# Kernel optimization log

Hardware: AMD Instinct MI355X
Metric: run time of the kernel (lower is better)

Reference implementation:

```python
import jax, jax.numpy as jnp
import numpy as np

SIZE = 11
SIGMA = 1.5
PAD = 5

def _window2d():
    # cv2.getGaussianKernel(11, 1.5): normalized 1D Gaussian, outer product -> 2D window
    x = np.arange(SIZE) - (SIZE - 1) / 2.0
    g = np.exp(-(x * x) / (2.0 * SIGMA * SIGMA))
    g = g / g.sum()
    return jnp.asarray(np.outer(g, g), dtype=jnp.float32)

def _gconv(x, w):
    # x: [H, W]; replicate ('edge') pad by 5 then valid 11x11 correlation (matches torch
    # Conv2d with padding_mode='replicate'); output [H, W]
    xp = jnp.pad(x, PAD, mode='edge')[None, None]  # [1,1,H+10,W+10]
    y = jax.lax.conv_general_dilated(
        xp, w[None, None], window_strides=(1, 1), padding='VALID',
        dimension_numbers=('NCHW', 'OIHW', 'NCHW'))
    return y[0, 0]

def setup_inputs() -> dict:
    key = jax.random.key(0)
    k1, k2 = jax.random.split(key)
    H = W = 4096
    img1 = jax.random.uniform(k1, (H, W), dtype=jnp.float32) * 255.0
    img2 = jax.random.uniform(k2, (H, W), dtype=jnp.float32) * 255.0
    return {"img1": img1, "img2": img2}

def reference(img1, img2):
    w = _window2d()
    C1 = (0.01 * 255) ** 2
    C2 = (0.03 * 255) ** 2
    mu1 = _gconv(img1, w)
    mu2 = _gconv(img2, w)
    mu1_sq = mu1 * mu1
    mu2_sq = mu2 * mu2
    mu1_mu2 = mu1 * mu2
    sigma1_sq = _gconv(img1 * img1, w) - mu1_sq
    sigma2_sq = _gconv(img2 * img2, w) - mu2_sq
    sigma12 = _gconv(img1 * img2, w) - mu1_mu2
    ssim_map = (2 * mu1_mu2 + C1) * (2 * sigma12 + C2) / (
        (mu1_sq + mu2_sq + C1) * (sigma1_sq + sigma2_sq + C2))
    return jnp.mean(ssim_map)
```

## Files before the change

kernel.cpp:

```cpp
#include <hip/hip_runtime.h>
#include <cmath>

#define IMG_H 4096
#define IMG_W 4096
#define GX 8
#define GY 128
#define TCOLS 512
#define WCOLS 128
#define R 32
#define NITER (R + 10)
#define GOUT ((NITER + 10) / 11)
#define SWORDS_W 144
#define NF4W 36
#define NSLOTW (2*NF4W)

struct GW { float w[11]; };

__device__ __forceinline__ int clampi(int v, int lo, int hi) {
  return v < lo ? lo : (v > hi ? hi : v);
}

__global__ __launch_bounds__(256, 2) void ssim_sweep_kernel(
    const float* __restrict__ img1, const float* __restrict__ img2,
    float* __restrict__ partial, GW gw) {
  __shared__ __align__(16) float sbuf[4][2][2][SWORDS_W];

  const int tid  = threadIdx.x;
  const int wv   = tid >> 6;
  const int lane = tid & 63;
  const int bx = blockIdx.x, by = blockIdx.y;
  const int cw   = bx * TCOLS + wv * WCOLS;
  const int row0 = by * R;
  const bool edge = (cw == 0) || (cw + WCOLS == IMG_W);

  const int  j0   = lane;
  const bool has2 = (lane < NSLOTW - 64);
  const int  j1   = lane + 64;

  auto load_slot = [&](int j, int gr) -> float4 {
    const float* img = (j < NF4W) ? img1 : img2;
    int wo = ((j < NF4W) ? j : j - NF4W) * 4;
    long rowbase = (long)gr * IMG_W;
    int gc = cw - 8 + wo;
    if (!edge) {
      return *reinterpret_cast<const float4*>(img + rowbase + gc);
    } else {
      float4 v;
      v.x = img[rowbase + clampi(gc + 0, 0, IMG_W - 1)];
      v.y = img[rowbase + clampi(gc + 1, 0, IMG_W - 1)];
      v.z = img[rowbase + clampi(gc + 2, 0, IMG_W - 1)];
      v.w = img[rowbase + clampi(gc + 3, 0, IMG_W - 1)];
      return v;
    }
  };
  auto store_slot = [&](int buf, int j, float4 v) {
    int im = (j < NF4W) ? 0 : 1;
    int wo = ((j < NF4W) ? j : j - NF4W) * 4;
    *reinterpret_cast<float4*>(&sbuf[wv][buf][im][wo]) = v;
  };

  {
    int gr = clampi(row0 - 5, 0, IMG_H - 1);
    float4 v0 = load_slot(j0, gr);
    store_slot(0, j0, v0);
    if (has2) { float4 v1 = load_slot(j1, gr); store_slot(0, j1, v1); }
  }

  float acc[4][11][2];
  float sum = 0.f;
  const float C1 = 6.5025f, C2 = 58.5225f;
  const int base = 2 * lane + 2;

  for (int g = 0; g < GOUT; ++g) {
    #pragma unroll
    for (int p = 0; p < 11; ++p) {
      const int i = g * 11 + p;
      if (i < NITER) {
        float4 pre0, pre1;
        const bool pf = (i + 1 < NITER);
        if (pf) {
          int gr = clampi(row0 - 5 + i + 1, 0, IMG_H - 1);
          pre0 = load_slot(j0, gr);
          if (has2) pre1 = load_slot(j1, gr);
        }

        const int cur = i & 1;
        float wa[14], wb[14];
        #pragma unroll
        for (int m = 0; m < 7; ++m) {
          float2 fa = *reinterpret_cast<const float2*>(&sbuf[wv][cur][0][base + 2 * m]);
          float2 fb = *reinterpret_cast<const float2*>(&sbuf[wv][cur][1][base + 2 * m]);
          wa[2 * m] = fa.x; wa[2 * m + 1] = fa.y;
          wb[2 * m] = fb.x; wb[2 * m + 1] = fb.y;
        }

        float h[4][2];
        #pragma unroll
        for (int ch = 0; ch < 4; ++ch) { h[ch][0] = 0.f; h[ch][1] = 0.f; }
        #pragma unroll
        for (int e = 1; e <= 12; ++e) {
          const float a = wa[e], b = wb[e];
          const float sq = fmaf(b, b, a * a);
          const float ab = a * b;
          if (e <= 11) {
            const float w0 = gw.w[e - 1];
            h[0][0] = fmaf(w0, a,  h[0][0]);
            h[1][0] = fmaf(w0, b,  h[1][0]);
            h[2][0] = fmaf(w0, sq, h[2][0]);
            h[3][0] = fmaf(w0, ab, h[3][0]);
          }
          if (e >= 2) {
            const float w1 = gw.w[e - 2];
            h[0][1] = fmaf(w1, a,  h[0][1]);
            h[1][1] = fmaf(w1, b,  h[1][1]);
            h[2][1] = fmaf(w1, sq, h[2][1]);
            h[3][1] = fmaf(w1, ab, h[3][1]);
          }
        }

        #pragma unroll
        for (int m = 0; m <= 10; ++m) {
          const int s = (p + 1 + m) % 11;
          const float wd = gw.w[10 - m];
          if (m == 10) {
            #pragma unroll
            for (int ch = 0; ch < 4; ++ch) {
              acc[ch][s][0] = wd * h[ch][0];
              acc[ch][s][1] = wd * h[ch][1];
            }
          } else {
            #pragma unroll
            for (int ch = 0; ch < 4; ++ch) {
              acc[ch][s][0] = fmaf(wd, h[ch][0], acc[ch][s][0]);
              acc[ch][s][1] = fmaf(wd, h[ch][1], acc[ch][s][1]);
            }
          }
        }

        if (i >= 10) {
          const int cs = (p + 1) % 11;
          #pragma unroll
          for (int x = 0; x < 2; ++x) {
            float mu1 = acc[0][cs][x], mu2 = acc[1][cs][x];
            float s3  = acc[2][cs][x], s4  = acc[3][cs][x];
            float mu1s = mu1 * mu1, mu2s = mu2 * mu2, m12 = mu1 * mu2;
            float num = (2.f * m12 + C1) * (2.f * (s4 - m12) + C2);
            float den = (mu1s + mu2s + C1) * ((s3 - mu1s - mu2s) + C2);
            sum += num * __builtin_amdgcn_rcpf(den);
          }
        }

        if (pf) {
          store_slot((i + 1) & 1, j0, pre0);
          if (has2) store_slot((i + 1) & 1, j1, pre1);
        }
      }
    }
  }

  #pragma unroll
  for (int off = 32; off > 0; off >>= 1) sum += __shfl_down(sum, off);
  __shared__ float wsum[4];
  if (lane == 0) wsum[wv] = sum;
  __syncthreads();
  if (tid == 0)
    partial[by * GX + bx] = wsum[0] + wsum[1] + wsum[2] + wsum[3];
}

__global__ __launch_bounds__(256) void ssim_reduce_kernel(
    const float* __restrict__ partial, float* __restrict__ out) {
  int tid = threadIdx.x;
  double s = (double)partial[tid] + (double)partial[tid + 256] +
             (double)partial[tid + 512] + (double)partial[tid + 768];
  #pragma unroll
  for (int off = 32; off > 0; off >>= 1) s += __shfl_down(s, off);
  __shared__ double ws[4];
  if ((tid & 63) == 0) ws[tid >> 6] = s;
  __syncthreads();
  if (tid == 0)
    out[0] = (float)((ws[0] + ws[1] + ws[2] + ws[3]) /
                     ((double)IMG_H * (double)IMG_W));
}

extern "C" void kernel_launch(void* const* d_in, const int* in_sizes, int n_in,
                              void* d_out, int out_size, void* d_ws, size_t ws_size,
                              hipStream_t stream) {
  const float* img1 = (const float*)d_in[0];
  const float* img2 = (const float*)d_in[1];
  float* partial = (float*)d_ws;
  float* out = (float*)d_out;

  GW gw;
  double g[11], s = 0.0;
  for (int i = 0; i < 11; ++i) {
    double x = i - 5.0;
    g[i] = exp(-(x * x) / (2.0 * 1.5 * 1.5));
    s += g[i];
  }
  for (int i = 0; i < 11; ++i) gw.w[i] = (float)(g[i] / s);

  dim3 grid(GX, GY);
  ssim_sweep_kernel<<<grid, 256, 0, stream>>>(img1, img2, partial, gw);
  ssim_reduce_kernel<<<1, 256, 0, stream>>>(partial, out);
}
```

Before: 200.8 us.

## Stage rows via direct global-to-LDS loads with triple buffering and taller row strips

Replaces register-staged float4 loads plus LDS stores with __builtin_amdgcn_global_load_lds into a three-deep per-wave ring, waited on with explicit vmcnt. Edge replication moves from per-element clamped global loads to an in-LDS fixup on edge wavefronts. Row strips double from 32 to 64 rows, so the 10-row halo is reloaded less often, with half as many blocks and a smaller final reduction. This aims to cut VGPR pressure and LDS store instructions and to keep loads in flight further ahead. The risks are fewer blocks, which lowers parallelism, and the hand-written vmcnt waits and missing LDS fences, which could race.

```diff
diff --git a/kernel.cpp b/kernel.cpp
--- a/kernel.cpp
+++ b/kernel.cpp
@@ -4,15 +4,15 @@
 #define IMG_H 4096
 #define IMG_W 4096
 #define GX 8
-#define GY 128
+#define GY 64
 #define TCOLS 512
 #define WCOLS 128
-#define R 32
+#define R 64
 #define NITER (R + 10)
 #define GOUT ((NITER + 10) / 11)
-#define SWORDS_W 144
-#define NF4W 36
-#define NSLOTW (2*NF4W)
+#define SW 144
+#define RWORDS (2*SW)
+#define NBUF 3
 
 struct GW { float w[11]; };
 
@@ -23,7 +23,7 @@
 __global__ __launch_bounds__(256, 2) void ssim_sweep_kernel(
     const float* __restrict__ img1, const float* __restrict__ img2,
     float* __restrict__ partial, GW gw) {
-  __shared__ __align__(16) float sbuf[4][2][2][SWORDS_W];
+  __shared__ __align__(16) float sbuf[4][NBUF][RWORDS];
 
   const int tid  = threadIdx.x;
   const int wv   = tid >> 6;
@@ -31,40 +31,32 @@
   const int bx = blockIdx.x, by = blockIdx.y;
   const int cw   = bx * TCOLS + wv * WCOLS;
   const int row0 = by * R;
-  const bool edge = (cw == 0) || (cw + WCOLS == IMG_W);
-
-  const int  j0   = lane;
-  const bool has2 = (lane < NSLOTW - 64);
-  const int  j1   = lane + 64;
-
-  auto load_slot = [&](int j, int gr) -> float4 {
-    const float* img = (j < NF4W) ? img1 : img2;
-    int wo = ((j < NF4W) ? j : j - NF4W) * 4;
-    long rowbase = (long)gr * IMG_W;
-    int gc = cw - 8 + wo;
-    if (!edge) {
-      return *reinterpret_cast<const float4*>(img + rowbase + gc);
-    } else {
-      float4 v;
-      v.x = img[rowbase + clampi(gc + 0, 0, IMG_W - 1)];
-      v.y = img[rowbase + clampi(gc + 1, 0, IMG_W - 1)];
-      v.z = img[rowbase + clampi(gc + 2, 0, IMG_W - 1)];
-      v.w = img[rowbase + clampi(gc + 3, 0, IMG_W - 1)];
-      return v;
+  const bool ledge = (cw == 0), redge = (cw + WCOLS == IMG_W);
+
+  const int   jjA   = (lane < 36) ? lane : lane - 36;
+  const float* baseA = (lane < 36) ? img1 : img2;
+  const int   coA   = clampi(cw - 8 + 4 * jjA, 0, IMG_W - 4);
+  const int   coB   = clampi(cw - 8 + 4 * (lane + 28), 0, IMG_W - 4);
+
+  float* swv = &sbuf[wv][0][0];
+
+  auto stage = [&](int i) {
+    const int b  = i % NBUF;
+    const int gr = clampi(row0 - 5 + i, 0, IMG_H - 1);
+    const long rb = (long)gr * IMG_W;
+    float* dst = swv + b * RWORDS;
+    __builtin_amdgcn_global_load_lds(
+        (const __attribute__((address_space(1))) void*)(baseA + rb + coA),
+        (__attribute__((address_space(3))) void*)dst, 16, 0, 0);
+    if (lane < 8) {
+      __builtin_amdgcn_global_load_lds(
+          (const __attribute__((address_space(1))) void*)(img2 + rb + coB),
+          (__attribute__((address_space(3))) void*)(dst + 256), 16, 0, 0);
     }
   };
-  auto store_slot = [&](int buf, int j, float4 v) {
-    int im = (j < NF4W) ? 0 : 1;
-    int wo = ((j < NF4W) ? j : j - NF4W) * 4;
-    *reinterpret_cast<float4*>(&sbuf[wv][buf][im][wo]) = v;
-  };
-
-  {
-    int gr = clampi(row0 - 5, 0, IMG_H - 1);
-    float4 v0 = load_slot(j0, gr);
-    store_slot(0, j0, v0);
-    if (has2) { float4 v1 = load_slot(j1, gr); store_slot(0, j1, v1); }
-  }
+
+  stage(0);
+  stage(1);
 
   float acc[4][11][2];
   float sum = 0.f;
@@ -76,20 +68,33 @@
     for (int p = 0; p < 11; ++p) {
       const int i = g * 11 + p;
       if (i < NITER) {
-        float4 pre0, pre1;
-        const bool pf = (i + 1 < NITER);
-        if (pf) {
-          int gr = clampi(row0 - 5 + i + 1, 0, IMG_H - 1);
-          pre0 = load_slot(j0, gr);
-          if (has2) pre1 = load_slot(j1, gr);
-        }
-
-        const int cur = i & 1;
+        if (i + 2 < NITER) stage(i + 2);
+
+        if (i + 2 < NITER) {
+          asm volatile("s_waitcnt vmcnt(4)" ::: "memory");
+        } else if (i + 1 < NITER) {
+          asm volatile("s_waitcnt vmcnt(2)" ::: "memory");
+        } else {
+          asm volatile("s_waitcnt vmcnt(0)" ::: "memory");
+        }
+        __builtin_amdgcn_sched_barrier(0);
+
+        float* buf = swv + (i % NBUF) * RWORDS;
+
+        if (ledge || redge) {
+          if (lane < 16) {
+            const int im = lane >> 3, l = lane & 7;
+            const int srcw = im * SW + (ledge ? 8 : 135);
+            const int dstw = im * SW + (ledge ? l : 136 + l);
+            buf[dstw] = buf[srcw];
+          }
+        }
+
         float wa[14], wb[14];
         #pragma unroll
         for (int m = 0; m < 7; ++m) {
-          float2 fa = *reinterpret_cast<const float2*>(&sbuf[wv][cur][0][base + 2 * m]);
-          float2 fb = *reinterpret_cast<const float2*>(&sbuf[wv][cur][1][base + 2 * m]);
+          float2 fa = *reinterpret_cast<const float2*>(&buf[base + 2 * m]);
+          float2 fb = *reinterpret_cast<const float2*>(&buf[SW + base + 2 * m]);
           wa[2 * m] = fa.x; wa[2 * m + 1] = fa.y;
           wb[2 * m] = fb.x; wb[2 * m + 1] = fb.y;
         }
@@ -149,11 +154,6 @@
             sum += num * __builtin_amdgcn_rcpf(den);
           }
         }
-
-        if (pf) {
-          store_slot((i + 1) & 1, j0, pre0);
-          if (has2) store_slot((i + 1) & 1, j1, pre1);
-        }
       }
     }
   }
@@ -170,8 +170,7 @@
 __global__ __launch_bounds__(256) void ssim_reduce_kernel(
     const float* __restrict__ partial, float* __restrict__ out) {
   int tid = threadIdx.x;
-  double s = (double)partial[tid] + (double)partial[tid + 256] +
-             (double)partial[tid + 512] + (double)partial[tid + 768];
+  double s = (double)partial[tid] + (double)partial[tid + 256];
   #pragma unroll
   for (int off = 32; off > 0; off >>= 1) s += __shfl_down(s, off);
   __shared__ double ws[4];
```

After: 202.0 us. Within noise of the previous version (+0.6%).
